# Performance work log

Measured on AMD Instinct MI355X. Metric: run time of the kernel, lower is better.

The kernel has to match this reference:

```python
import jax, jax.numpy as jnp
import numpy as np

RADIUS = 8
EPSILON = 0.01


def _diff_x(x, r):
    left = x[..., r:2 * r + 1, :]
    middle = x[..., 2 * r + 1:, :] - x[..., :-2 * r - 1, :]
    right = x[..., -1:, :] - x[..., -2 * r - 1:-r - 1, :]
    return jnp.concatenate([left, middle, right], axis=-2)


def _diff_y(x, r):
    left = x[..., r:2 * r + 1]
    middle = x[..., 2 * r + 1:] - x[..., :-2 * r - 1]
    right = x[..., -1:] - x[..., -2 * r - 1:-r - 1]
    return jnp.concatenate([left, middle, right], axis=-1)


def box_filter(x, r):
    # x: (N, C, H, W) -> windowed mean over (2r+1)x(2r+1) with reflect padding
    x = jnp.pad(x, ((0, 0), (0, 0), (r, r), (r, r)), mode='reflect')
    x = jnp.cumsum(x, axis=-2)
    x = _diff_x(x, r)
    x = jnp.cumsum(x, axis=-1)
    x = _diff_y(x, r)
    return x[..., r:-r, r:-r] / float((2 * r + 1) ** 2)


def setup_inputs() -> dict:
    key = jax.random.key(0)
    k1, k2 = jax.random.split(key)
    B, C, H, W = 4, 3, 1024, 1024
    I = jax.random.uniform(k1, (B, C, H, W), dtype=jnp.float32)
    p = jax.random.uniform(k2, (B, 1, H, W), dtype=jnp.float32)
    return {"I": I, "p": p}


def reference(I, p) -> jnp.ndarray:
    r, eps = RADIUS, EPSILON
    B, C, H, W = I.shape

    mean_I = box_filter(I, r)                     # (B,C,H,W)
    mean_p = box_filter(p, r)                     # (B,1,H,W)
    mean_Ip = box_filter(I * p, r)                # (B,C,H,W)
    cov_Ip = mean_Ip - mean_I * mean_p            # (B,C,H,W)

    # second moments: (B,C,C,H,W) via reshape to (B*C, C, H, W) for the box filter
    II = I[:, :, None] * I[:, None]               # (B,C,C,H,W)
    mean_II = box_filter(II.reshape(B * C, C, H, W), r).reshape(B, C, C, H, W)
    cov_II = mean_II - mean_I[:, :, None] * mean_I[:, None]

    eye = jnp.eye(C, dtype=I.dtype).reshape(1, C, C, 1, 1)
    S = cov_II + eps * eye                        # (B,C,C,H,W)

    # per-pixel CxC solve: move pixel dims to batch
    S_px = jnp.transpose(S, (0, 3, 4, 1, 2))      # (B,H,W,C,C)
    rhs = jnp.transpose(cov_Ip, (0, 2, 3, 1))[..., None]  # (B,H,W,C,1)
    a = jnp.linalg.solve(S_px, rhs)[..., 0]       # (B,H,W,C)
    a = jnp.transpose(a, (0, 3, 1, 2))            # (B,C,H,W)

    a_mean_I = jnp.einsum('bchw,bchw->bhw', a, mean_I)
    b = mean_p - a_mean_I[:, None]                # (B,1,H,W)

    mean_a = box_filter(a, r)
    mean_b = box_filter(b, r)

    q = jnp.einsum('bchw,bchw->bhw', mean_a, I) + mean_b[:, 0]
    return q[:, None]                             # (B,1,H,W)
```

## Files before the change

### kernel.cpp

```cpp
#include <hip/hip_runtime.h>

#define HH 1024
#define WW 1024
#define NB 4
#define RR 8
#define NCH1 13
#define NCH2 4
#define NXCD 8
#define VSEG1 4
#define NSEG1 (HH / VSEG1)
#define NBLK1 (NB * NSEG1)
#define LDSW1 1040
#define VSEG2 8
#define NSEG2 (HH / VSEG2)
#define TW 512
#define NBLK2 (NB * NSEG2 * 2)
#define LDSW2 544
#define INV_AREA (1.0f/289.0f)
#define EPS_REG 0.01f

typedef float f4 __attribute__((ext_vector_type(4)));
typedef _Float16 h4 __attribute__((ext_vector_type(4)));
typedef float f2 __attribute__((ext_vector_type(2)));
typedef _Float16 h2 __attribute__((ext_vector_type(2)));

__device__ __forceinline__ int refl(int j, int n) {
    int k = j < 0 ? -j : j;
    return k >= n ? 2 * n - 2 - k : k;
}

__device__ __forceinline__ void derived13(f4 i0, f4 i1, f4 i2, f4 pp, f4* d) {
    d[0] = i0; d[1] = i1; d[2] = i2; d[3] = pp;
    d[4] = i0 * pp; d[5] = i1 * pp; d[6] = i2 * pp;
    d[7] = i0 * i0; d[8] = i0 * i1; d[9] = i0 * i2;
    d[10] = i1 * i1; d[11] = i1 * i2; d[12] = i2 * i2;
}


__global__ __launch_bounds__(256, 3) void gf_stage1(
    const float* __restrict__ I, const float* __restrict__ P,
    _Float16* __restrict__ A, _Float16* __restrict__ Bc)
{
    __shared__ float lds[NCH1][LDSW1];
    const int tid = threadIdx.x;
    const int xcd = blockIdx.x & (NXCD - 1);
    const int rank = blockIdx.x >> 3;
    const int bz = xcd >> 1;
    const int seg = (xcd & 1) * 128 + rank;
    const int y0 = seg * VSEG1;
    const int c0 = 4 * tid;
    const float* Ib = I + (size_t)bz * 3 * HH * WW;
    const float* Pb = P + (size_t)bz * HH * WW;

    f4 vs[NCH1];
    #pragma unroll
    for (int ch = 0; ch < NCH1; ++ch) { vs[ch] = (f4){0.f, 0.f, 0.f, 0.f}; }

    for (int dy = -RR; dy <= RR; ++dy) {
        int row = refl(y0 + dy, HH);
        size_t rb = (size_t)row * WW + c0;
        f4 i0 = *(const f4*)(Ib + rb);
        f4 i1 = *(const f4*)(Ib + (size_t)HH * WW + rb);
        f4 i2 = *(const f4*)(Ib + (size_t)2 * HH * WW + rb);
        f4 pp = *(const f4*)(Pb + rb);
        f4 d[NCH1]; derived13(i0, i1, i2, pp, d);
        #pragma unroll
        for (int ch = 0; ch < NCH1; ++ch) vs[ch] += d[ch];
    }

    for (int y = y0; y < y0 + VSEG1; ++y) {
        #pragma unroll
        for (int ch = 0; ch < NCH1; ++ch)
            *(f4*)&lds[ch][8 + c0] = vs[ch];
        if (tid <= 2) {
            #pragma unroll
            for (int j = 0; j < 4; ++j) {
                int c = c0 + j;
                if (c >= 1 && c <= 8) {
                    #pragma unroll
                    for (int ch = 0; ch < NCH1; ++ch) lds[ch][8 - c] = vs[ch][j];
                }
            }
        }
        if (tid >= 253) {
            #pragma unroll
            for (int j = 0; j < 4; ++j) {
                int c = c0 + j;
                if (c >= 1015 && c <= 1022) {
                    #pragma unroll
                    for (int ch = 0; ch < NCH1; ++ch) lds[ch][1032 + (1022 - c)] = vs[ch][j];
                }
            }
        }
        __syncthreads();

        f4 m[NCH1];
        #pragma unroll
        for (int ch = 0; ch < NCH1; ++ch) {
            float vv[20];
            #pragma unroll
            for (int k = 0; k < 5; ++k)
                ((f4*)vv)[k] = *(const f4*)&lds[ch][c0 + 4 * k];
            float s = (((vv[0]+vv[1])+(vv[2]+vv[3])) + ((vv[4]+vv[5])+(vv[6]+vv[7])))
                    + (((vv[8]+vv[9])+(vv[10]+vv[11])) + ((vv[12]+vv[13])+(vv[14]+vv[15])))
                    + vv[16];
            f4 mm;
            mm[0] = s;
            s += vv[17] - vv[0]; mm[1] = s;
            s += vv[18] - vv[1]; mm[2] = s;
            s += vv[19] - vv[2]; mm[3] = s;
            m[ch] = mm * INV_AREA;
        }

        f4 oa0, oa1, oa2, ob;
        #pragma unroll
        for (int j = 0; j < 4; ++j) {
            float m0 = m[0][j], m1 = m[1][j], m2 = m[2][j], m3 = m[3][j];
            float r0 = m[4][j] - m0 * m3;
            float r1 = m[5][j] - m1 * m3;
            float r2 = m[6][j] - m2 * m3;
            float S00 = m[7][j]  - m0 * m0 + EPS_REG;
            float S01 = m[8][j]  - m0 * m1;
            float S02 = m[9][j]  - m0 * m2;
            float S11 = m[10][j] - m1 * m1 + EPS_REG;
            float S12 = m[11][j] - m1 * m2;
            float S22 = m[12][j] - m2 * m2 + EPS_REG;
            float A0 = S11 * S22 - S12 * S12;
            float B0 = S02 * S12 - S01 * S22;
            float C0 = S01 * S12 - S02 * S11;
            float D0 = S00 * S22 - S02 * S02;
            float E0 = S01 * S02 - S00 * S12;
            float F0 = S00 * S11 - S01 * S01;
            float det = S00 * A0 + S01 * B0 + S02 * C0;
            float inv = 1.0f / det;
            float a0 = (A0 * r0 + B0 * r1 + C0 * r2) * inv;
            float a1 = (B0 * r0 + D0 * r1 + E0 * r2) * inv;
            float a2 = (C0 * r0 + E0 * r1 + F0 * r2) * inv;
            float bb = m3 - (a0 * m0 + a1 * m1 + a2 * m2);
            oa0[j] = a0; oa1[j] = a1; oa2[j] = a2; ob[j] = bb;
        }
        size_t obase = (size_t)y * WW + c0;
        *(h4*)(A + (size_t)(bz * 3 + 0) * HH * WW + obase) = __builtin_convertvector(oa0, h4);
        *(h4*)(A + (size_t)(bz * 3 + 1) * HH * WW + obase) = __builtin_convertvector(oa1, h4);
        *(h4*)(A + (size_t)(bz * 3 + 2) * HH * WW + obase) = __builtin_convertvector(oa2, h4);
        *(h4*)(Bc + (size_t)bz * HH * WW + obase) = __builtin_convertvector(ob, h4);
        __syncthreads();

        if (y + 1 < y0 + VSEG1) {
            int ra = refl(y + 1 + RR, HH);
            int rs = refl(y - RR, HH);
            size_t rba = (size_t)ra * WW + c0;
            size_t rbs = (size_t)rs * WW + c0;
            f4 ai0 = *(const f4*)(Ib + rba);
            f4 ai1 = *(const f4*)(Ib + (size_t)HH * WW + rba);
            f4 ai2 = *(const f4*)(Ib + (size_t)2 * HH * WW + rba);
            f4 ap  = *(const f4*)(Pb + rba);
            f4 d[NCH1];
            derived13(ai0, ai1, ai2, ap, d);
            #pragma unroll
            for (int ch = 0; ch < NCH1; ++ch) vs[ch] += d[ch];
            f4 si0 = *(const f4*)(Ib + rbs);
            f4 si1 = *(const f4*)(Ib + (size_t)HH * WW + rbs);
            f4 si2 = *(const f4*)(Ib + (size_t)2 * HH * WW + rbs);
            f4 sp  = *(const f4*)(Pb + rbs);
            derived13(si0, si1, si2, sp, d);
            #pragma unroll
            for (int ch = 0; ch < NCH1; ++ch) vs[ch] -= d[ch];
        }
    }
}

__device__ __forceinline__ f2 hwin2(const float* ldsrow, int c0) {
    const f2* wp = (const f2*)(ldsrow + c0);
    f2 w0 = wp[0], w1 = wp[1], w2 = wp[2], w3 = wp[3];
    f2 w4 = wp[4], w5 = wp[5], w6 = wp[6], w7 = wp[7], w8 = wp[8];
    f2 e = ((w0 + w1) + (w2 + w3)) + ((w4 + w5) + (w6 + w7));
    float s0 = e[0] + e[1] + w8[0];
    float s1 = s0 - w0[0] + w8[1];
    f2 r; r[0] = s0 * INV_AREA; r[1] = s1 * INV_AREA;
    return r;
}

__global__ __launch_bounds__(256, 2) void gf_stage2(
    const float* __restrict__ I, const _Float16* __restrict__ A,
    const _Float16* __restrict__ Bc, float* __restrict__ Q)
{
    __shared__ float lds[NCH2][LDSW2];
    const int tid = threadIdx.x;
    const int xcd = blockIdx.x & (NXCD - 1);
    const int rank = blockIdx.x >> 3;
    const int bz = xcd >> 1;
    const int seg = (xcd & 1) * 64 + (rank >> 1);
    const int y0 = seg * VSEG2;
    const int wstart = (rank & 1) * TW;
    const int c0 = 2 * tid;
    const int gc = wstart + c0;
    const _Float16* A0p = A + (size_t)(bz * 3 + 0) * HH * WW;
    const _Float16* A1p = A + (size_t)(bz * 3 + 1) * HH * WW;
    const _Float16* A2p = A + (size_t)(bz * 3 + 2) * HH * WW;
    const _Float16* Bp  = Bc + (size_t)bz * HH * WW;
    const float* Ib  = I + (size_t)bz * 3 * HH * WW;

    const bool isHalo = tid < 16;
    const int hraw = (tid < 8) ? (wstart - 8 + tid) : (wstart + TW + (tid - 8));
    const int hg = refl(hraw, WW);
    const int hpos = (tid < 8) ? tid : (8 + TW + (tid - 8));

    f2 vs[NCH2];
    float hs[NCH2];
    #pragma unroll
    for (int ch = 0; ch < NCH2; ++ch) { vs[ch] = (f2){0.f, 0.f}; hs[ch] = 0.f; }

    for (int dy = -RR; dy <= RR; ++dy) {
        int row = refl(y0 + dy, HH);
        size_t rb = (size_t)row * WW;
        vs[0] += __builtin_convertvector(*(const h2*)(A0p + rb + gc), f2);
        vs[1] += __builtin_convertvector(*(const h2*)(A1p + rb + gc), f2);
        vs[2] += __builtin_convertvector(*(const h2*)(A2p + rb + gc), f2);
        vs[3] += __builtin_convertvector(*(const h2*)(Bp + rb + gc), f2);
        if (isHalo) {
            hs[0] += (float)A0p[rb + hg];
            hs[1] += (float)A1p[rb + hg];
            hs[2] += (float)A2p[rb + hg];
            hs[3] += (float)Bp[rb + hg];
        }
    }

    for (int y = y0; y < y0 + VSEG2; ++y) {
        #pragma unroll
        for (int ch = 0; ch < NCH2; ++ch)
            *(f2*)&lds[ch][8 + c0] = vs[ch];
        if (isHalo) {
            #pragma unroll
            for (int ch = 0; ch < NCH2; ++ch) lds[ch][hpos] = hs[ch];
        }
        const bool upd = (y + 1 < y0 + VSEG2);
        f2 aa0, aa1, aa2, ab, sa0, sa1, sa2, sb;
        float ha0, ha1, ha2, hab, hb0, hb1, hb2, hbb;
        size_t rbq = (size_t)y * WW;
        f2 i0 = *(const f2*)(Ib + rbq + gc);
        f2 i1 = *(const f2*)(Ib + (size_t)HH * WW + rbq + gc);
        f2 i2 = *(const f2*)(Ib + (size_t)2 * HH * WW + rbq + gc);
        if (upd) {
            int ra = refl(y + 1 + RR, HH);
            int rs = refl(y - RR, HH);
            size_t rba = (size_t)ra * WW;
            size_t rbs = (size_t)rs * WW;
            aa0 = __builtin_convertvector(*(const h2*)(A0p + rba + gc), f2);
            aa1 = __builtin_convertvector(*(const h2*)(A1p + rba + gc), f2);
            aa2 = __builtin_convertvector(*(const h2*)(A2p + rba + gc), f2);
            ab  = __builtin_convertvector(*(const h2*)(Bp + rba + gc), f2);
            sa0 = __builtin_convertvector(*(const h2*)(A0p + rbs + gc), f2);
            sa1 = __builtin_convertvector(*(const h2*)(A1p + rbs + gc), f2);
            sa2 = __builtin_convertvector(*(const h2*)(A2p + rbs + gc), f2);
            sb  = __builtin_convertvector(*(const h2*)(Bp + rbs + gc), f2);
            if (isHalo) {
                ha0 = (float)A0p[rba + hg]; ha1 = (float)A1p[rba + hg];
                ha2 = (float)A2p[rba + hg]; hab = (float)Bp[rba + hg];
                hb0 = (float)A0p[rbs + hg]; hb1 = (float)A1p[rbs + hg];
                hb2 = (float)A2p[rbs + hg]; hbb = (float)Bp[rbs + hg];
            }
        }
        __syncthreads();

        f2 m[NCH2];
        #pragma unroll
        for (int ch = 0; ch < NCH2; ++ch)
            m[ch] = hwin2(&lds[ch][0], c0);

        f2 qv = m[0] * i0 + m[1] * i1 + m[2] * i2 + m[3];
        *(f2*)(Q + (size_t)bz * HH * WW + rbq + gc) = qv;
        __syncthreads();

        if (upd) {
            vs[0] += aa0 - sa0;
            vs[1] += aa1 - sa1;
            vs[2] += aa2 - sa2;
            vs[3] += ab - sb;
            if (isHalo) {
                hs[0] += ha0 - hb0; hs[1] += ha1 - hb1;
                hs[2] += ha2 - hb2; hs[3] += hab - hbb;
            }
        }
    }
}

extern "C" void kernel_launch(void* const* d_in, const int* in_sizes, int n_in,
                              void* d_out, int out_size, void* d_ws, size_t ws_size,
                              hipStream_t stream) {
    const float* I = (const float*)d_in[0];
    const float* P = (const float*)d_in[1];
    float* Q = (float*)d_out;
    _Float16* A = (_Float16*)d_ws;
    _Float16* Bc = A + (size_t)NB * 3 * HH * WW;
    gf_stage1<<<NBLK1, 256, 0, stream>>>(I, P, A, Bc);
    gf_stage2<<<NBLK2, 256, 0, stream>>>(I, A, Bc, Q);
}
```

Before: 82.61 us.

## Split stage1 into single-wave 256-column strips with halo columns to drop barriers

```diff
diff --git a/kernel.cpp b/kernel.cpp
--- a/kernel.cpp
+++ b/kernel.cpp
@@ -7,14 +7,12 @@
 #define NCH1 13
 #define NCH2 4
 #define NXCD 8
-#define VSEG1 4
-#define NSEG1 (HH / VSEG1)
-#define NBLK1 (NB * NSEG1)
-#define LDSW1 1040
+#define VSEG1 8
+#define NBLK1 (NB * (HH / VSEG1) * 4)
+#define PADW 276
 #define VSEG2 8
-#define NSEG2 (HH / VSEG2)
 #define TW 512
-#define NBLK2 (NB * NSEG2 * 2)
+#define NBLK2 (NB * (HH / VSEG2) * 2)
 #define LDSW2 544
 #define INV_AREA (1.0f/289.0f)
 #define EPS_REG 0.01f
@@ -36,63 +34,73 @@
     d[10] = i1 * i1; d[11] = i1 * i2; d[12] = i2 * i2;
 }
 
-
-__global__ __launch_bounds__(256, 3) void gf_stage1(
+__device__ __forceinline__ void derived13s(float i0, float i1, float i2, float pp, float* d) {
+    d[0] = i0; d[1] = i1; d[2] = i2; d[3] = pp;
+    d[4] = i0 * pp; d[5] = i1 * pp; d[6] = i2 * pp;
+    d[7] = i0 * i0; d[8] = i0 * i1; d[9] = i0 * i2;
+    d[10] = i1 * i1; d[11] = i1 * i2; d[12] = i2 * i2;
+}
+
+
+__global__ __launch_bounds__(64, 2) void gf_stage1(
     const float* __restrict__ I, const float* __restrict__ P,
     _Float16* __restrict__ A, _Float16* __restrict__ Bc)
 {
-    __shared__ float lds[NCH1][LDSW1];
-    const int tid = threadIdx.x;
+    __shared__ float lds[NCH1][PADW];
+    const int lane = threadIdx.x;
     const int xcd = blockIdx.x & (NXCD - 1);
     const int rank = blockIdx.x >> 3;
     const int bz = xcd >> 1;
-    const int seg = (xcd & 1) * 128 + rank;
+    const int strip = rank & 3;
+    const int seg = (xcd & 1) * 64 + (rank >> 2);
     const int y0 = seg * VSEG1;
-    const int c0 = 4 * tid;
+    const int wb = strip * 256;
+    const int cm = wb + 4 * lane;
     const float* Ib = I + (size_t)bz * 3 * HH * WW;
     const float* Pb = P + (size_t)bz * HH * WW;
 
+    const bool isH = lane < 16;
+    const int hloc = (lane < 8) ? lane : (264 + lane - 8);
+    const int hraw = (lane < 8) ? (wb - 8 + lane) : (wb + 256 + (lane - 8));
+    const int hg = refl(hraw, WW);
+
     f4 vs[NCH1];
     #pragma unroll
-    for (int ch = 0; ch < NCH1; ++ch) { vs[ch] = (f4){0.f, 0.f, 0.f, 0.f}; }
-
-    for (int dy = -RR; dy <= RR; ++dy) {
-        int row = refl(y0 + dy, HH);
-        size_t rb = (size_t)row * WW + c0;
-        f4 i0 = *(const f4*)(Ib + rb);
-        f4 i1 = *(const f4*)(Ib + (size_t)HH * WW + rb);
-        f4 i2 = *(const f4*)(Ib + (size_t)2 * HH * WW + rb);
-        f4 pp = *(const f4*)(Pb + rb);
-        f4 d[NCH1]; derived13(i0, i1, i2, pp, d);
-        #pragma unroll
-        for (int ch = 0; ch < NCH1; ++ch) vs[ch] += d[ch];
+    for (int ch = 0; ch < NCH1; ++ch) vs[ch] = (f4){0.f, 0.f, 0.f, 0.f};
+    {
+        float hs[NCH1];
+        #pragma unroll
+        for (int ch = 0; ch < NCH1; ++ch) hs[ch] = 0.f;
+        for (int dy = -RR; dy <= RR; ++dy) {
+            int row = refl(y0 + dy, HH);
+            size_t rb = (size_t)row * WW;
+            f4 i0 = *(const f4*)(Ib + rb + cm);
+            f4 i1 = *(const f4*)(Ib + (size_t)HH * WW + rb + cm);
+            f4 i2 = *(const f4*)(Ib + (size_t)2 * HH * WW + rb + cm);
+            f4 pp = *(const f4*)(Pb + rb + cm);
+            f4 d[NCH1]; derived13(i0, i1, i2, pp, d);
+            #pragma unroll
+            for (int ch = 0; ch < NCH1; ++ch) vs[ch] += d[ch];
+            if (isH) {
+                float j0 = Ib[rb + hg];
+                float j1 = Ib[(size_t)HH * WW + rb + hg];
+                float j2 = Ib[(size_t)2 * HH * WW + rb + hg];
+                float jp = Pb[rb + hg];
+                float ds[NCH1]; derived13s(j0, j1, j2, jp, ds);
+                #pragma unroll
+                for (int ch = 0; ch < NCH1; ++ch) hs[ch] += ds[ch];
+            }
+        }
+        if (isH) {
+            #pragma unroll
+            for (int ch = 0; ch < NCH1; ++ch) lds[ch][hloc] = hs[ch];
+        }
     }
 
     for (int y = y0; y < y0 + VSEG1; ++y) {
         #pragma unroll
         for (int ch = 0; ch < NCH1; ++ch)
-            *(f4*)&lds[ch][8 + c0] = vs[ch];
-        if (tid <= 2) {
-            #pragma unroll
-            for (int j = 0; j < 4; ++j) {
-                int c = c0 + j;
-                if (c >= 1 && c <= 8) {
-                    #pragma unroll
-                    for (int ch = 0; ch < NCH1; ++ch) lds[ch][8 - c] = vs[ch][j];
-                }
-            }
-        }
-        if (tid >= 253) {
-            #pragma unroll
-            for (int j = 0; j < 4; ++j) {
-                int c = c0 + j;
-                if (c >= 1015 && c <= 1022) {
-                    #pragma unroll
-                    for (int ch = 0; ch < NCH1; ++ch) lds[ch][1032 + (1022 - c)] = vs[ch][j];
-                }
-            }
-        }
-        __syncthreads();
+            *(f4*)&lds[ch][8 + 4 * lane] = vs[ch];
 
         f4 m[NCH1];
         #pragma unroll
@@ -100,7 +108,7 @@
             float vv[20];
             #pragma unroll
             for (int k = 0; k < 5; ++k)
-                ((f4*)vv)[k] = *(const f4*)&lds[ch][c0 + 4 * k];
+                ((f4*)vv)[k] = *(const f4*)&lds[ch][4 * lane + 4 * k];
             float s = (((vv[0]+vv[1])+(vv[2]+vv[3])) + ((vv[4]+vv[5])+(vv[6]+vv[7])))
                     + (((vv[8]+vv[9])+(vv[10]+vv[11])) + ((vv[12]+vv[13])+(vv[14]+vv[15])))
                     + vv[16];
@@ -139,33 +147,51 @@
             float bb = m3 - (a0 * m0 + a1 * m1 + a2 * m2);
             oa0[j] = a0; oa1[j] = a1; oa2[j] = a2; ob[j] = bb;
         }
-        size_t obase = (size_t)y * WW + c0;
+        size_t obase = (size_t)y * WW + cm;
         *(h4*)(A + (size_t)(bz * 3 + 0) * HH * WW + obase) = __builtin_convertvector(oa0, h4);
         *(h4*)(A + (size_t)(bz * 3 + 1) * HH * WW + obase) = __builtin_convertvector(oa1, h4);
         *(h4*)(A + (size_t)(bz * 3 + 2) * HH * WW + obase) = __builtin_convertvector(oa2, h4);
         *(h4*)(Bc + (size_t)bz * HH * WW + obase) = __builtin_convertvector(ob, h4);
-        __syncthreads();
 
         if (y + 1 < y0 + VSEG1) {
             int ra = refl(y + 1 + RR, HH);
             int rs = refl(y - RR, HH);
-            size_t rba = (size_t)ra * WW + c0;
-            size_t rbs = (size_t)rs * WW + c0;
-            f4 ai0 = *(const f4*)(Ib + rba);
-            f4 ai1 = *(const f4*)(Ib + (size_t)HH * WW + rba);
-            f4 ai2 = *(const f4*)(Ib + (size_t)2 * HH * WW + rba);
-            f4 ap  = *(const f4*)(Pb + rba);
-            f4 d[NCH1];
-            derived13(ai0, ai1, ai2, ap, d);
-            #pragma unroll
-            for (int ch = 0; ch < NCH1; ++ch) vs[ch] += d[ch];
-            f4 si0 = *(const f4*)(Ib + rbs);
-            f4 si1 = *(const f4*)(Ib + (size_t)HH * WW + rbs);
-            f4 si2 = *(const f4*)(Ib + (size_t)2 * HH * WW + rbs);
-            f4 sp  = *(const f4*)(Pb + rbs);
-            derived13(si0, si1, si2, sp, d);
-            #pragma unroll
-            for (int ch = 0; ch < NCH1; ++ch) vs[ch] -= d[ch];
+            size_t rba = (size_t)ra * WW;
+            size_t rbs = (size_t)rs * WW;
+            {
+                f4 i0 = *(const f4*)(Ib + rba + cm);
+                f4 i1 = *(const f4*)(Ib + (size_t)HH * WW + rba + cm);
+                f4 i2 = *(const f4*)(Ib + (size_t)2 * HH * WW + rba + cm);
+                f4 pp = *(const f4*)(Pb + rba + cm);
+                f4 d[NCH1]; derived13(i0, i1, i2, pp, d);
+                #pragma unroll
+                for (int ch = 0; ch < NCH1; ++ch) vs[ch] += d[ch];
+            }
+            {
+                f4 i0 = *(const f4*)(Ib + rbs + cm);
+                f4 i1 = *(const f4*)(Ib + (size_t)HH * WW + rbs + cm);
+                f4 i2 = *(const f4*)(Ib + (size_t)2 * HH * WW + rbs + cm);
+                f4 pp = *(const f4*)(Pb + rbs + cm);
+                f4 d[NCH1]; derived13(i0, i1, i2, pp, d);
+                #pragma unroll
+                for (int ch = 0; ch < NCH1; ++ch) vs[ch] -= d[ch];
+            }
+            if (isH) {
+                float a0v = Ib[rba + hg];
+                float a1v = Ib[(size_t)HH * WW + rba + hg];
+                float a2v = Ib[(size_t)2 * HH * WW + rba + hg];
+                float apv = Pb[rba + hg];
+                float s0v = Ib[rbs + hg];
+                float s1v = Ib[(size_t)HH * WW + rbs + hg];
+                float s2v = Ib[(size_t)2 * HH * WW + rbs + hg];
+                float spv = Pb[rbs + hg];
+                float dA[NCH1], dS[NCH1];
+                derived13s(a0v, a1v, a2v, apv, dA);
+                derived13s(s0v, s1v, s2v, spv, dS);
+                #pragma unroll
+                for (int ch = 0; ch < NCH1; ++ch)
+                    lds[ch][hloc] += dA[ch] - dS[ch];
+            }
         }
     }
 }
@@ -293,6 +319,6 @@
     float* Q = (float*)d_out;
     _Float16* A = (_Float16*)d_ws;
     _Float16* Bc = A + (size_t)NB * 3 * HH * WW;
-    gf_stage1<<<NBLK1, 256, 0, stream>>>(I, P, A, Bc);
+    gf_stage1<<<NBLK1, 64, 0, stream>>>(I, P, A, Bc);
     gf_stage2<<<NBLK2, 256, 0, stream>>>(I, A, Bc, Q);
 }
```

Measured after the change: 85.65 us. 3.7% more time.
